# Kernel tuning notes

Hardware: AMD Instinct MI355X
Metric: run time of the kernel (lower is better)

Reference implementation:

```python
import jax, jax.numpy as jnp
import numpy as np

B, T, H = 128, 2048, 128

def setup_inputs() -> dict:
    key = jax.random.key(0)
    k1, k2, k3, k4, k5, k6 = jax.random.split(key, 6)
    s = 1.0 / np.sqrt(H)
    return {
        "H_pos": jax.random.normal(k1, (B, T, H), jnp.float32),
        "H_dyn": jax.random.normal(k2, (B, T, H), jnp.float32),
        "acc_w": jax.random.uniform(k3, (B, T), jnp.float32),
        "W_h": jax.random.uniform(k4, (H, H), jnp.float32, -s, s),
        "W_d": jax.random.uniform(k5, (H, H), jnp.float32, -s, s),
        "W_a": jax.random.uniform(k6, (H,), jnp.float32, -s, s),
        "b_a": jnp.zeros((), jnp.float32),
        "beta": jnp.zeros((), jnp.float32),
    }

def reference(H_pos, H_dyn, acc_w, W_h, W_d, W_a, b_a, beta):
    # energy: W_a(tanh(W_h H_pos + W_d H_dyn)) -> [B, T]
    z = jnp.tanh(jnp.einsum('bth,oh->bto', H_pos, W_h)
                 + jnp.einsum('bth,oh->bto', H_dyn, W_d))
    energy = jnp.einsum('bth,h->bt', z, W_a) + b_a
    # acceleration normalization
    acc_norm = acc_w / jnp.clip(jnp.max(acc_w, axis=1, keepdims=True), 1e-6)
    beta_pos = jax.nn.softplus(beta)
    alpha = jax.nn.softmax(energy * (1.0 + beta_pos * acc_norm), axis=1)  # [B, T]
    context = jnp.einsum('bt,bth->bh', alpha, H_pos)  # [B, H]
    return (context, alpha)
```

## Files before the change

### kernel.cpp

```cpp
#include <hip/hip_runtime.h>

#define B_ 128
#define T_ 2048
#define H_ 128
#define WPAD 136

typedef __attribute__((ext_vector_type(8))) short short8;
typedef __attribute__((ext_vector_type(4))) float f32x4;

__device__ __forceinline__ unsigned short f2b(float f) {
    unsigned int u = __float_as_uint(f);
    u += 0x7fffu + ((u >> 16) & 1u);
    return (unsigned short)(u >> 16);
}
__device__ __forceinline__ short8 pack8(const float4 x, const float4 y) {
    short8 r;
    r[0] = (short)f2b(x.x); r[1] = (short)f2b(x.y);
    r[2] = (short)f2b(x.z); r[3] = (short)f2b(x.w);
    r[4] = (short)f2b(y.x); r[5] = (short)f2b(y.y);
    r[6] = (short)f2b(y.z); r[7] = (short)f2b(y.w);
    return r;
}
__device__ __forceinline__ float tanh_fast(float x) {
    x = fminf(fmaxf(x, -20.f), 20.f);
    float e = __expf(2.f * x);
    return (e - 1.f) / (e + 1.f);
}

__global__ __launch_bounds__(512) void energy_kernel(
    const float* __restrict__ Hp,
    const float* __restrict__ Hd,
    const float* __restrict__ Wh,
    const float* __restrict__ Wd,
    const float* __restrict__ Wa,
    const float* __restrict__ ba_p,
    float* __restrict__ energy,
    int ntiles)
{
    __shared__ unsigned short Whs[H_ * WPAD];
    __shared__ unsigned short Wds[H_ * WPAD];
    __shared__ float Was[H_];

    const int tid = threadIdx.x;

    for (int i = tid; i < (H_ * H_) / 4; i += 512) {
        int row = i >> 5;
        int c4  = (i & 31) * 4;
        float4 wh = *(const float4*)&Wh[row * H_ + c4];
        float4 wd = *(const float4*)&Wd[row * H_ + c4];
        uint2 ph, pd;
        ph.x = (unsigned)f2b(wh.x) | ((unsigned)f2b(wh.y) << 16);
        ph.y = (unsigned)f2b(wh.z) | ((unsigned)f2b(wh.w) << 16);
        pd.x = (unsigned)f2b(wd.x) | ((unsigned)f2b(wd.y) << 16);
        pd.y = (unsigned)f2b(wd.z) | ((unsigned)f2b(wd.w) << 16);
        *(uint2*)&Whs[row * WPAD + c4] = ph;
        *(uint2*)&Wds[row * WPAD + c4] = pd;
    }
    if (tid < H_) Was[tid] = Wa[tid];
    __syncthreads();

    const float ba = ba_p[0];

    const int wave = tid >> 6;
    const int lane = tid & 63;
    const int l15  = lane & 15;
    const int lq   = lane >> 4;

    for (int tile = blockIdx.x; tile < ntiles; tile += gridDim.x) {
        const int row_base = tile * 128 + wave * 16;
        const float* ap = Hp + (size_t)(row_base + l15) * H_ + lq * 8;
        const float* ad = Hd + (size_t)(row_base + l15) * H_ + lq * 8;

        f32x4 acc[8];
        #pragma unroll
        for (int nt = 0; nt < 8; nt++) acc[nt] = (f32x4){0.f, 0.f, 0.f, 0.f};

        float4 cx0 = *(const float4*)(ap);
        float4 cx1 = *(const float4*)(ap + 4);

        #pragma unroll 1
        for (int kt = 0; kt < 8; kt++) {
            float4 nx0 = cx0, nx1 = cx1;
            if (kt < 7) {
                int ktn = kt + 1;
                const float* pn = (ktn < 4) ? (ap + ktn * 32) : (ad + (ktn - 4) * 32);
                nx0 = *(const float4*)pn;
                nx1 = *(const float4*)(pn + 4);
            }
            short8 af = pack8(cx0, cx1);
            const unsigned short* ws = (kt < 4) ? Whs : Wds;
            const int kk = (kt & 3) * 32 + lq * 8;
            #pragma unroll
            for (int nt = 0; nt < 8; nt++) {
                short8 bf = *(const short8*)&ws[(nt * 16 + l15) * WPAD + kk];
                acc[nt] = __builtin_amdgcn_mfma_f32_16x16x32_bf16(af, bf, acc[nt], 0, 0, 0);
            }
            cx0 = nx0; cx1 = nx1;
        }

        float ep[4] = {0.f, 0.f, 0.f, 0.f};
        #pragma unroll
        for (int nt = 0; nt < 8; nt++) {
            const float wa = Was[nt * 16 + l15];
            #pragma unroll
            for (int r = 0; r < 4; r++) ep[r] += tanh_fast(acc[nt][r]) * wa;
        }
        #pragma unroll
        for (int m = 1; m < 16; m <<= 1) {
            #pragma unroll
            for (int r = 0; r < 4; r++) ep[r] += __shfl_xor(ep[r], m, 64);
        }
        if (l15 == 0) {
            #pragma unroll
            for (int r = 0; r < 4; r++)
                energy[row_base + lq * 4 + r] = ep[r] + ba;
        }
    }
}

__global__ __launch_bounds__(256) void softmax_ctx_kernel(
    const float* __restrict__ Hp,
    const float* __restrict__ accw,
    const float* __restrict__ beta_p,
    const float* __restrict__ energy,
    float* __restrict__ out_alpha,
    float* __restrict__ cpart)
{
    __shared__ float al_s[T_];
    __shared__ float red[8 * H_];
    __shared__ float sred[8];

    const int sl   = blockIdx.x & 7;
    const int b    = blockIdx.x >> 3;
    const int tid  = threadIdx.x;
    const int lane = tid & 63;
    const int wid  = tid >> 6;

    const float beta_pos = log1pf(__expf(beta_p[0]));

    float av[8], ev[8];
    {
        const float* pa = accw + b * T_ + tid * 8;
        const float* pe = energy + b * T_ + tid * 8;
        float4 a0 = *(const float4*)pa, a1 = *(const float4*)(pa + 4);
        float4 e0 = *(const float4*)pe, e1 = *(const float4*)(pe + 4);
        av[0]=a0.x; av[1]=a0.y; av[2]=a0.z; av[3]=a0.w;
        av[4]=a1.x; av[5]=a1.y; av[6]=a1.z; av[7]=a1.w;
        ev[0]=e0.x; ev[1]=e0.y; ev[2]=e0.z; ev[3]=e0.w;
        ev[4]=e1.x; ev[5]=e1.y; ev[6]=e1.z; ev[7]=e1.w;
    }
    float amax = -1e30f;
    #pragma unroll
    for (int i = 0; i < 8; i++) amax = fmaxf(amax, av[i]);
    for (int m = 32; m >= 1; m >>= 1) amax = fmaxf(amax, __shfl_xor(amax, m, 64));
    if (lane == 0) sred[wid] = amax;
    __syncthreads();
    if (tid == 0)
        sred[4] = fmaxf(fmaxf(sred[0], sred[1]), fmaxf(sred[2], sred[3]));
    __syncthreads();
    const float invd = beta_pos / fmaxf(sred[4], 1e-6f);

    float sv[8], smax = -1e30f;
    #pragma unroll
    for (int i = 0; i < 8; i++) {
        sv[i] = ev[i] * (1.f + av[i] * invd);
        smax = fmaxf(smax, sv[i]);
    }
    for (int m = 32; m >= 1; m >>= 1) smax = fmaxf(smax, __shfl_xor(smax, m, 64));
    __syncthreads();
    if (lane == 0) sred[wid] = smax;
    __syncthreads();
    if (tid == 0)
        sred[5] = fmaxf(fmaxf(sred[0], sred[1]), fmaxf(sred[2], sred[3]));
    __syncthreads();
    const float smax_all = sred[5];

    float p[8], psum = 0.f;
    #pragma unroll
    for (int i = 0; i < 8; i++) { p[i] = __expf(sv[i] - smax_all); psum += p[i]; }
    for (int m = 32; m >= 1; m >>= 1) psum += __shfl_xor(psum, m, 64);
    __syncthreads();
    if (lane == 0) sred[wid] = psum;
    __syncthreads();
    if (tid == 0)
        sred[6] = sred[0] + sred[1] + sred[2] + sred[3];
    __syncthreads();
    const float invS = 1.f / sred[6];

    #pragma unroll
    for (int i = 0; i < 8; i++) al_s[tid * 8 + i] = p[i] * invS;
    __syncthreads();

    out_alpha[b * T_ + sl * 256 + tid] = al_s[sl * 256 + tid];

    const int row = tid >> 5;
    const int c4  = tid & 31;

    float c0 = 0.f, c1 = 0.f, c2 = 0.f, c3 = 0.f;
    const float* base = Hp + ((size_t)b * T_ + sl * 256) * H_ + c4 * 4;
    const float* al   = al_s + sl * 256;
    #pragma unroll 4
    for (int it = 0; it < 32; it++) {
        int t = it * 8 + row;
        float a = al[t];
        float4 v = *(const float4*)(base + (size_t)t * H_);
        c0 += a * v.x; c1 += a * v.y; c2 += a * v.z; c3 += a * v.w;
    }
    red[row * H_ + c4 * 4 + 0] = c0;
    red[row * H_ + c4 * 4 + 1] = c1;
    red[row * H_ + c4 * 4 + 2] = c2;
    red[row * H_ + c4 * 4 + 3] = c3;
    __syncthreads();
    if (tid < H_) {
        float s = 0.f;
        #pragma unroll
        for (int g = 0; g < 8; g++) s += red[g * H_ + tid];
        cpart[(b * 8 + sl) * H_ + tid] = s;
    }
}

__global__ __launch_bounds__(256) void ctx_reduce_kernel(
    const float* __restrict__ cpart, float* __restrict__ out_ctx)
{
    int i = blockIdx.x * 256 + threadIdx.x;
    if (i < B_ * H_) {
        int b = i >> 7, h = i & 127;
        float s = 0.f;
        #pragma unroll
        for (int g = 0; g < 8; g++) s += cpart[(b * 8 + g) * H_ + h];
        out_ctx[i] = s;
    }
}

extern "C" void kernel_launch(void* const* d_in, const int* in_sizes, int n_in,
                              void* d_out, int out_size, void* d_ws, size_t ws_size,
                              hipStream_t stream) {
    const float* Hp   = (const float*)d_in[0];
    const float* Hd   = (const float*)d_in[1];
    const float* accw = (const float*)d_in[2];
    const float* Wh   = (const float*)d_in[3];
    const float* Wd   = (const float*)d_in[4];
    const float* Wa   = (const float*)d_in[5];
    const float* ba   = (const float*)d_in[6];
    const float* beta = (const float*)d_in[7];

    float* energy_ws = (float*)d_ws;
    float* cpart_ws  = energy_ws + B_ * T_;

    float* out_ctx   = (float*)d_out;
    float* out_alpha = out_ctx + B_ * H_;

    const int ntiles = (B_ * T_) / 128;
    energy_kernel<<<512, 512, 0, stream>>>(Hp, Hd, Wh, Wd, Wa, ba, energy_ws, ntiles);
    softmax_ctx_kernel<<<B_ * 8, 256, 0, stream>>>(Hp, accw, beta, energy_ws, out_alpha, cpart_ws);
    ctx_reduce_kernel<<<(B_ * H_ + 255) / 256, 256, 0, stream>>>(cpart_ws, out_ctx);
}
```

Baseline: 320.5 us.

## Prefetch next tile's activations in registers and pre-swizzle weights in LDS

The energy kernel now holds a full tile's worth of activation fragments (16 float4 per lane) in registers. It loads the next tile's fragments while computing the current one, replacing the old one-k-step lookahead with a whole-tile software pipeline. The loop over k is fully unrolled. The weights are stored in LDS in an MFMA-fragment-ordered layout, so each lane reads contiguous 16 bytes at lane*8 with a constant offset, which removes the padded indexing. The cost is much higher register pressure, which may lower occupancy. On the last tile the prefetch redundantly reloads the same addresses.

```diff
diff --git a/kernel.cpp b/kernel.cpp
--- a/kernel.cpp
+++ b/kernel.cpp
@@ -3,7 +3,6 @@
 #define B_ 128
 #define T_ 2048
 #define H_ 128
-#define WPAD 136
 
 typedef __attribute__((ext_vector_type(8))) short short8;
 typedef __attribute__((ext_vector_type(4))) float f32x4;
@@ -37,24 +36,30 @@
     float* __restrict__ energy,
     int ntiles)
 {
-    __shared__ unsigned short Whs[H_ * WPAD];
-    __shared__ unsigned short Wds[H_ * WPAD];
+    __shared__ unsigned short Wpack[8 * 8 * 64 * 8];
     __shared__ float Was[H_];
 
     const int tid = threadIdx.x;
 
     for (int i = tid; i < (H_ * H_) / 4; i += 512) {
-        int row = i >> 5;
-        int c4  = (i & 31) * 4;
-        float4 wh = *(const float4*)&Wh[row * H_ + c4];
-        float4 wd = *(const float4*)&Wd[row * H_ + c4];
-        uint2 ph, pd;
-        ph.x = (unsigned)f2b(wh.x) | ((unsigned)f2b(wh.y) << 16);
-        ph.y = (unsigned)f2b(wh.z) | ((unsigned)f2b(wh.w) << 16);
-        pd.x = (unsigned)f2b(wd.x) | ((unsigned)f2b(wd.y) << 16);
-        pd.y = (unsigned)f2b(wd.z) | ((unsigned)f2b(wd.w) << 16);
-        *(uint2*)&Whs[row * WPAD + c4] = ph;
-        *(uint2*)&Wds[row * WPAD + c4] = pd;
+        int o  = i >> 5;
+        int c4 = i & 31;
+        float4 wh = *(const float4*)&Wh[o * H_ + c4 * 4];
+        float4 wd = *(const float4*)&Wd[o * H_ + c4 * 4];
+        uint2 ph, pdv;
+        ph.x  = (unsigned)f2b(wh.x) | ((unsigned)f2b(wh.y) << 16);
+        ph.y  = (unsigned)f2b(wh.z) | ((unsigned)f2b(wh.w) << 16);
+        pdv.x = (unsigned)f2b(wd.x) | ((unsigned)f2b(wd.y) << 16);
+        pdv.y = (unsigned)f2b(wd.z) | ((unsigned)f2b(wd.w) << 16);
+        int nt   = o >> 4;
+        int l15  = o & 15;
+        int kth  = c4 >> 3;
+        int lq   = (c4 >> 1) & 3;
+        int half = (c4 & 1) * 4;
+        int bh = ((kth * 8 + nt) * 64 + lq * 16 + l15) * 8 + half;
+        int bd = (((kth + 4) * 8 + nt) * 64 + lq * 16 + l15) * 8 + half;
+        *(uint2*)&Wpack[bh] = ph;
+        *(uint2*)&Wpack[bd] = pdv;
     }
     if (tid < H_) Was[tid] = Wa[tid];
     __syncthreads();
@@ -66,36 +71,42 @@
     const int l15  = lane & 15;
     const int lq   = lane >> 4;
 
+    const unsigned short* wb = Wpack + lane * 8;
+
+    const size_t estep = (size_t)gridDim.x * 128 * H_;
+
+    const int row0 = blockIdx.x * 128 + wave * 16;
+    const float* pp = Hp + (size_t)(row0 + l15) * H_ + lq * 8;
+    const float* pd = Hd + (size_t)(row0 + l15) * H_ + lq * 8;
+
+    float4 abuf[16];
+    #pragma unroll
+    for (int kt = 0; kt < 8; kt++) {
+        const float* s = (kt < 4) ? (pp + kt * 32) : (pd + (kt - 4) * 32);
+        abuf[2 * kt]     = *(const float4*)s;
+        abuf[2 * kt + 1] = *(const float4*)(s + 4);
+    }
+
     for (int tile = blockIdx.x; tile < ntiles; tile += gridDim.x) {
         const int row_base = tile * 128 + wave * 16;
-        const float* ap = Hp + (size_t)(row_base + l15) * H_ + lq * 8;
-        const float* ad = Hd + (size_t)(row_base + l15) * H_ + lq * 8;
+        const size_t adv = (tile + (int)gridDim.x < ntiles) ? estep : 0;
+        pp += adv; pd += adv;
 
         f32x4 acc[8];
         #pragma unroll
         for (int nt = 0; nt < 8; nt++) acc[nt] = (f32x4){0.f, 0.f, 0.f, 0.f};
 
-        float4 cx0 = *(const float4*)(ap);
-        float4 cx1 = *(const float4*)(ap + 4);
-
-        #pragma unroll 1
+        #pragma unroll
         for (int kt = 0; kt < 8; kt++) {
-            float4 nx0 = cx0, nx1 = cx1;
-            if (kt < 7) {
-                int ktn = kt + 1;
-                const float* pn = (ktn < 4) ? (ap + ktn * 32) : (ad + (ktn - 4) * 32);
-                nx0 = *(const float4*)pn;
-                nx1 = *(const float4*)(pn + 4);
-            }
-            short8 af = pack8(cx0, cx1);
-            const unsigned short* ws = (kt < 4) ? Whs : Wds;
-            const int kk = (kt & 3) * 32 + lq * 8;
+            short8 af = pack8(abuf[2 * kt], abuf[2 * kt + 1]);
+            const float* s = (kt < 4) ? (pp + kt * 32) : (pd + (kt - 4) * 32);
+            abuf[2 * kt]     = *(const float4*)s;
+            abuf[2 * kt + 1] = *(const float4*)(s + 4);
             #pragma unroll
             for (int nt = 0; nt < 8; nt++) {
-                short8 bf = *(const short8*)&ws[(nt * 16 + l15) * WPAD + kk];
+                short8 bf = *(const short8*)(wb + kt * 4096 + nt * 512);
                 acc[nt] = __builtin_amdgcn_mfma_f32_16x16x32_bf16(af, bf, acc[nt], 0, 0, 0);
             }
-            cx0 = nx0; cx1 = nx1;
         }
 
         float ep[4] = {0.f, 0.f, 0.f, 0.f};
```

Measured after the change: 400.0 us. +24.8%, slower.
